# Kernel optimization log

Measured on AMD Instinct MI355X. Metric: run time of the kernel, lower is better.

The kernel has to match this reference:

```python
import jax, jax.numpy as jnp
import numpy as np

K = 3        # kernel_size
STRIDE = 1
PAD = 1
OUT_H = 64
OUT_W = 64


def _unfold(x):
    """torch.nn.Unfold equivalent: x (B,C,H,W) -> patches (B, L, C*K*K),
    feature index ordered c*K*K + ki*K + kj (channel-major, like torch)."""
    B, C, H, W = x.shape
    xp = jnp.pad(x, ((0, 0), (0, 0), (PAD, PAD), (PAD, PAD)))
    # gather K*K shifted views; loop is over the small fixed kernel window only
    rows = []
    for ki in range(K):
        cols = []
        for kj in range(K):
            cols.append(xp[:, :, ki:ki + STRIDE * OUT_H:STRIDE,
                               kj:kj + STRIDE * OUT_W:STRIDE])  # (B,C,oh,ow)
        rows.append(jnp.stack(cols, axis=2))  # (B,C,K,oh,ow)
    p = jnp.stack(rows, axis=2)               # (B,C,K,K,oh,ow)
    # -> (B, oh, ow, C, K, K) -> (B, L, C*K*K)
    p = p.transpose(0, 4, 5, 1, 2, 3)
    return p.reshape(B, OUT_H * OUT_W, C * K * K)


def setup_inputs() -> dict:
    key = jax.random.key(0)
    k1, k2, k3 = jax.random.split(key, 3)
    B, C = 16, 32
    out_ch = 64
    L = OUT_H * OUT_W                 # 4096
    in_feat = C * K * K               # 288
    x = jax.random.normal(k1, (B, C, 64, 64), dtype=jnp.float32)
    # kaiming_uniform with a=sqrt(5) on (in_feat, out_ch) slices -> bound = 1/sqrt(in_feat)
    bound = 1.0 / np.sqrt(in_feat)
    weight = jax.random.uniform(k2, (L, in_feat, out_ch), dtype=jnp.float32,
                                minval=-bound, maxval=bound)
    bias = jax.random.uniform(k3, (L, out_ch), dtype=jnp.float32,
                              minval=-bound, maxval=bound)
    return {"x": x, "weight": weight, "bias": bias}


def reference(x, weight, bias):
    B = x.shape[0]
    out_ch = weight.shape[-1]
    patches = _unfold(x)                               # (B, L, in_feat)
    out = jnp.einsum('bli,lio->blo', patches, weight)  # per-location matmul
    out = out + bias[None]                             # (B, L, out_ch)
    out = out.transpose(0, 2, 1).reshape(B, out_ch, OUT_H, OUT_W)
    return out
```

## Files before the change

kernel.cpp:

```cpp
#include <hip/hip_runtime.h>

#define L_TOT   4096
#define CIN     32
#define G_L     4
#define NROW    576
#define NSTAGE  96

#define FMA16(PP, WW) {                                                        \
    acc[0][0] += PP.x * WW.x; acc[0][1] += PP.x * WW.y;                        \
    acc[0][2] += PP.x * WW.z; acc[0][3] += PP.x * WW.w;                        \
    acc[1][0] += PP.y * WW.x; acc[1][1] += PP.y * WW.y;                        \
    acc[1][2] += PP.y * WW.z; acc[1][3] += PP.y * WW.w;                        \
    acc[2][0] += PP.z * WW.x; acc[2][1] += PP.z * WW.y;                        \
    acc[2][2] += PP.z * WW.z; acc[2][3] += PP.z * WW.w;                        \
    acc[3][0] += PP.w * WW.x; acc[3][1] += PP.w * WW.y;                        \
    acc[3][2] += PP.w * WW.z; acc[3][3] += PP.w * WW.w; }

#define WLOAD(BB, SS) {                                                        \
    BB[0] = wp[(3 * (SS) + 0) * 16];                                           \
    BB[1] = wp[(3 * (SS) + 1) * 16];                                           \
    BB[2] = wp[(3 * (SS) + 2) * 16]; }

#define STEP(BB, SS) {                                                         \
    const float* pr = xs + ((6 * (SS) + g) << 4) + (wv << 2);                  \
    float4 p0 = *(const float4*)(pr);                                          \
    float4 p1 = *(const float4*)(pr + 16);                                     \
    float4 p2 = *(const float4*)(pr + 32);                                     \
    FMA16(p0, BB[0]); FMA16(p1, BB[1]); FMA16(p2, BB[2]); }

__global__ __launch_bounds__(256, 4)
void lc2d_v3(const float* __restrict__ x,
             const float* __restrict__ weight,
             const float* __restrict__ bias,
             float* __restrict__ out) {
    __shared__ float xs[NROW * 16];

    const int tid  = threadIdx.x;
    const int lane = tid & 63;
    const int wv   = tid >> 6;
    const int g    = lane >> 4;
    const int o4   = lane & 15;
    const int l0   = blockIdx.x * G_L;
    const int oh   = l0 >> 6;
    const int ow0  = l0 & 63;

    for (int u = tid; u < 1536; u += 256) {
        int b  = u & 15;
        int t  = u >> 4;
        int dh = t % 3;
        int c  = t / 3;
        int h  = oh - 1 + dh;
        bool hok = (unsigned)h < 64u;
        const float* xrow = x + (((b * CIN + c) * 64 + h) << 6);
        int wbase = ow0 - 1;
#pragma unroll
        for (int wl = 0; wl < 6; ++wl) {
            int ww = wbase + wl;
            float v = (hok && (unsigned)ww < 64u) ? xrow[ww] : 0.0f;
            xs[(t * 6 + wl) * 16 + b] = v;
        }
    }
    __syncthreads();

    const float4* __restrict__ W4 = (const float4*)weight;
    const float4* wp = W4 + (size_t)(l0 + g) * (288 * 16) + o4;

    const float4 bias4 = ((const float4*)bias)[(l0 + g) * 16 + o4];
    float acc[4][4];
#pragma unroll
    for (int bq = 0; bq < 4; ++bq) {
        acc[bq][0] = bias4.x; acc[bq][1] = bias4.y;
        acc[bq][2] = bias4.z; acc[bq][3] = bias4.w;
    }

    float4 bA[3], bB[3], bC[3], bD[3];
    WLOAD(bA, 0); WLOAD(bB, 1); WLOAD(bC, 2);

    for (int t = 0; t < 23; ++t) {
        const int s = t * 4;
        WLOAD(bD, s + 3); STEP(bA, s);
        WLOAD(bA, s + 4); STEP(bB, s + 1);
        WLOAD(bB, s + 5); STEP(bC, s + 2);
        WLOAD(bC, s + 6); STEP(bD, s + 3);
    }
    WLOAD(bD, 95); STEP(bA, 92);
    STEP(bB, 93); STEP(bC, 94); STEP(bD, 95);

#pragma unroll
    for (int bq = 0; bq < 4; ++bq) {
        const int b = (wv << 2) + bq;
#pragma unroll
        for (int j = 0; j < 4; ++j) {
            out[((size_t)((b << 6) + (o4 << 2) + j) << 12) + l0 + g] = acc[bq][j];
        }
    }
}

extern "C" void kernel_launch(void* const* d_in, const int* in_sizes, int n_in,
                              void* d_out, int out_size, void* d_ws, size_t ws_size,
                              hipStream_t stream) {
    const float* x      = (const float*)d_in[0];
    const float* weight = (const float*)d_in[1];
    const float* bias   = (const float*)d_in[2];
    float* out          = (float*)d_out;

    dim3 grid(L_TOT / G_L);
    dim3 block(256);
    hipLaunchKernelGGL(lc2d_v3, grid, block, 0, stream, x, weight, bias, out);
}
```

Before: 457.7 us.

## Stage weights through double-buffered LDS using async global_load_lds

Instead of each wave loading the per-location weights from global memory into registers, the block asynchronously copies 4-stage chunks of weights into a double-buffered LDS region with global_load_lds. All four waves then read them from shared memory, while the next chunk is prefetched during compute. This removes the redundant global and cache traffic from the four waves reading identical weights. In exchange it adds a barrier per chunk, extra LDS use, and a lowered occupancy hint.

New measurement: 444.3 us. -2.9%, faster.

```diff
diff --git a/kernel.cpp b/kernel.cpp
--- a/kernel.cpp
+++ b/kernel.cpp
@@ -3,8 +3,12 @@
 #define L_TOT   4096
 #define CIN     32
 #define G_L     4
-#define NROW    576
-#define NSTAGE  96
+#define CH      4
+#define NCHUNK  24
+#define CHUNK_STRIDE_F (CH * 3 * 64)
+
+using f32g = __attribute__((address_space(1))) const float;
+using f32l = __attribute__((address_space(3))) float;
 
 #define FMA16(PP, WW) {                                                        \
     acc[0][0] += PP.x * WW.x; acc[0][1] += PP.x * WW.y;                        \
@@ -16,24 +20,13 @@
     acc[3][0] += PP.w * WW.x; acc[3][1] += PP.w * WW.y;                        \
     acc[3][2] += PP.w * WW.z; acc[3][3] += PP.w * WW.w; }
 
-#define WLOAD(BB, SS) {                                                        \
-    BB[0] = wp[(3 * (SS) + 0) * 16];                                           \
-    BB[1] = wp[(3 * (SS) + 1) * 16];                                           \
-    BB[2] = wp[(3 * (SS) + 2) * 16]; }
-
-#define STEP(BB, SS) {                                                         \
-    const float* pr = xs + ((6 * (SS) + g) << 4) + (wv << 2);                  \
-    float4 p0 = *(const float4*)(pr);                                          \
-    float4 p1 = *(const float4*)(pr + 16);                                     \
-    float4 p2 = *(const float4*)(pr + 32);                                     \
-    FMA16(p0, BB[0]); FMA16(p1, BB[1]); FMA16(p2, BB[2]); }
-
-__global__ __launch_bounds__(256, 4)
-void lc2d_v3(const float* __restrict__ x,
+__global__ __launch_bounds__(256, 2)
+void lc2d_v6(const float* __restrict__ x,
              const float* __restrict__ weight,
              const float* __restrict__ bias,
              float* __restrict__ out) {
-    __shared__ float xs[NROW * 16];
+    __shared__ __align__(16) float xs[576 * 16];
+    __shared__ __align__(16) float wsm[2][12 * 256];
 
     const int tid  = threadIdx.x;
     const int lane = tid & 63;
@@ -43,6 +36,22 @@
     const int l0   = blockIdx.x * G_L;
     const int oh   = l0 >> 6;
     const int ow0  = l0 & 63;
+
+    const float* gsrc[3];
+    int ldsoff[3];
+#pragma unroll
+    for (int t = 0; t < 3; ++t) {
+        int p   = wv + (t << 2);
+        int gg  = p / 3;
+        int sub = p - 3 * gg;
+        gsrc[t] = weight + (size_t)(l0 + gg) * (288 * 64) + sub * 256 + (lane << 2);
+        ldsoff[t] = p * 256;
+    }
+
+#pragma unroll
+    for (int t = 0; t < 3; ++t)
+        __builtin_amdgcn_global_load_lds((f32g*)(gsrc[t]),
+                                         (f32l*)(&wsm[0][ldsoff[t]]), 16, 0, 0);
 
     for (int u = tid; u < 1536; u += 256) {
         int b  = u & 15;
@@ -62,9 +71,6 @@
     }
     __syncthreads();
 
-    const float4* __restrict__ W4 = (const float4*)weight;
-    const float4* wp = W4 + (size_t)(l0 + g) * (288 * 16) + o4;
-
     const float4 bias4 = ((const float4*)bias)[(l0 + g) * 16 + o4];
     float acc[4][4];
 #pragma unroll
@@ -73,18 +79,41 @@
         acc[bq][2] = bias4.z; acc[bq][3] = bias4.w;
     }
 
-    float4 bA[3], bB[3], bC[3], bD[3];
-    WLOAD(bA, 0); WLOAD(bB, 1); WLOAD(bC, 2);
-
-    for (int t = 0; t < 23; ++t) {
-        const int s = t * 4;
-        WLOAD(bD, s + 3); STEP(bA, s);
-        WLOAD(bA, s + 4); STEP(bB, s + 1);
-        WLOAD(bB, s + 5); STEP(bC, s + 2);
-        WLOAD(bC, s + 6); STEP(bD, s + 3);
+    int buf = 0;
+    for (int k = 0; k < NCHUNK - 1; ++k) {
+#pragma unroll
+        for (int t = 0; t < 3; ++t)
+            __builtin_amdgcn_global_load_lds((f32g*)(gsrc[t] + (size_t)(k + 1) * CHUNK_STRIDE_F),
+                                             (f32l*)(&wsm[buf ^ 1][ldsoff[t]]), 16, 0, 0);
+#pragma unroll
+        for (int sl = 0; sl < CH; ++sl) {
+            const int s = (k << 2) + sl;
+            const float* pr = xs + ((6 * s + g) << 4) + (wv << 2);
+            float4 p0 = *(const float4*)(pr);
+            float4 p1 = *(const float4*)(pr + 16);
+            float4 p2 = *(const float4*)(pr + 32);
+            const float4* wr = (const float4*)&wsm[buf][0] + g * 192 + sl * 48 + o4;
+            float4 w0 = wr[0];
+            float4 w1 = wr[16];
+            float4 w2 = wr[32];
+            FMA16(p0, w0); FMA16(p1, w1); FMA16(p2, w2);
+        }
+        __syncthreads();
+        buf ^= 1;
     }
-    WLOAD(bD, 95); STEP(bA, 92);
-    STEP(bB, 93); STEP(bC, 94); STEP(bD, 95);
+#pragma unroll
+    for (int sl = 0; sl < CH; ++sl) {
+        const int s = ((NCHUNK - 1) << 2) + sl;
+        const float* pr = xs + ((6 * s + g) << 4) + (wv << 2);
+        float4 p0 = *(const float4*)(pr);
+        float4 p1 = *(const float4*)(pr + 16);
+        float4 p2 = *(const float4*)(pr + 32);
+        const float4* wr = (const float4*)&wsm[buf][0] + g * 192 + sl * 48 + o4;
+        float4 w0 = wr[0];
+        float4 w1 = wr[16];
+        float4 w2 = wr[32];
+        FMA16(p0, w0); FMA16(p1, w1); FMA16(p2, w2);
+    }
 
 #pragma unroll
     for (int bq = 0; bq < 4; ++bq) {
@@ -106,5 +135,5 @@
 
     dim3 grid(L_TOT / G_L);
     dim3 block(256);
-    hipLaunchKernelGGL(lc2d_v3, grid, block, 0, stream, x, weight, bias, out);
+    hipLaunchKernelGGL(lc2d_v6, grid, block, 0, stream, x, weight, bias, out);
 }
```
